# Optimization experiments

Measured on AMD Instinct MI355X. Metric: run time of the kernel, lower is better.

## Reference

```python
import jax, jax.numpy as jnp
import numpy as np

B, H, W, D, C = 2, 128, 128, 8, 64
HEADS, DIM_HEAD = 4, 16
F_IN = C * D            # 512
F_OUT = DIM_HEAD * HEADS * D  # 512


def setup_inputs() -> dict:
    key = jax.random.key(0)
    ks = jax.random.split(key, 8)
    s = 0.02
    return {
        "x_in": jax.random.normal(ks[0], (B, H, W, D, C), dtype=jnp.float32),
        "Wq": jax.random.normal(ks[1], (F_IN, F_OUT), dtype=jnp.float32) * s,
        "Wk": jax.random.normal(ks[2], (F_IN, F_OUT), dtype=jnp.float32) * s,
        "Wv": jax.random.normal(ks[3], (F_IN, F_OUT), dtype=jnp.float32) * s,
        "rescale": jnp.ones((HEADS, 1, 1), dtype=jnp.float32),
        "Wp": jax.random.normal(ks[4], (F_OUT, F_IN), dtype=jnp.float32) * s,
        "bp": jnp.zeros((F_IN,), dtype=jnp.float32),
        "pos_w1": jax.random.normal(ks[5], (C, 1, 3, 3, 3), dtype=jnp.float32) * s,
        "pos_w2": jax.random.normal(ks[6], (C, 1, 3, 3, 3), dtype=jnp.float32) * s,
    }


def _dwconv3d(y, kern, groups):
    # y: [b,c,d,h,w], kern: [c,1,3,3,3] depthwise
    return jax.lax.conv_general_dilated(
        y, kern, window_strides=(1, 1, 1), padding="SAME",
        feature_group_count=groups,
        dimension_numbers=("NCDHW", "OIDHW", "NCDHW"))


def reference(x_in, Wq, Wk, Wv, rescale, Wp, bp, pos_w1, pos_w2):
    b, h, w, d, c = x_in.shape
    heads = rescale.shape[0]
    n = h * w
    x = x_in.reshape(b, n, d * c)
    q_inp = x @ Wq
    k_inp = x @ Wk
    v_inp = x @ Wv

    def split(t):  # [b,n,heads*Dh] -> [b,heads,Dh,n]  (Dh = dim_head*num_frm)
        return t.reshape(b, n, heads, -1).transpose(0, 2, 3, 1)

    q, k, v = split(q_inp), split(k_inp), split(v_inp)
    # L2-normalize along spatial axis n (last dim), torch F.normalize eps=1e-12
    q = q / jnp.maximum(jnp.linalg.norm(q, axis=-1, keepdims=True), 1e-12)
    k = k / jnp.maximum(jnp.linalg.norm(k, axis=-1, keepdims=True), 1e-12)
    # channel attention: [b,heads,Dh,Dh]
    attn = jnp.einsum("bhdn,bhen->bhde", k, q) * rescale
    attn = jax.nn.softmax(attn, axis=-1)
    out = jnp.einsum("bhde,bhen->bhdn", attn, v)  # [b,heads,Dh,n]
    out = out.transpose(0, 3, 1, 2).reshape(b, n, -1)  # [b,n,heads*Dh]
    out_c = (out @ Wp + bp).reshape(b, h, w, d, c)

    # positional branch: depthwise conv3d over [b,c,d,h,w]
    vp = v_inp.reshape(b, h, w, d, c).transpose(0, 4, 3, 1, 2)
    p = _dwconv3d(vp, pos_w1, c)
    p = jax.nn.gelu(p, approximate=False)
    p = _dwconv3d(p, pos_w2, c)
    out_p = p.transpose(0, 3, 4, 2, 1)  # -> [b,h,w,d,c]
    return out_c + out_p
```

## Files before the change

### kernel.cpp

```cpp
#include <hip/hip_runtime.h>
#include <math.h>
#include <stdint.h>


using short8  = __attribute__((ext_vector_type(8))) short;
using f32x4   = __attribute__((ext_vector_type(4))) float;

__device__ __forceinline__ float bf2f(unsigned short u) {
  union { unsigned int i; float f; } v; v.i = ((unsigned int)u) << 16; return v.f;
}
__device__ __forceinline__ unsigned short f2bf(float f) {
  union { float f; unsigned int i; } v; v.f = f;
  unsigned int r = v.i + 0x7fffu + ((v.i >> 16) & 1u);
  return (unsigned short)(r >> 16);
}

__device__ __forceinline__ void g2l16(const void* g, void* l) {
  __builtin_amdgcn_global_load_lds(
      (__attribute__((address_space(1))) void*)(unsigned long long)(uintptr_t)g,
      (__attribute__((address_space(3))) void*)(unsigned int)(uintptr_t)l,
      16, 0, 0);
}

__global__ __launch_bounds__(256) void convert_x(const float* __restrict__ x,
                                                 unsigned short* __restrict__ xb) {
  int i = (blockIdx.x * 256 + threadIdx.x) * 4;
  float4 v = *(const float4*)&x[i];
  ushort4 o;
  o.x = f2bf(v.x); o.y = f2bf(v.y); o.z = f2bf(v.z); o.w = f2bf(v.w);
  *(ushort4*)&xb[i] = o;
}

__global__ __launch_bounds__(256) void prep_w(const float* __restrict__ Wq,
                                              const float* __restrict__ Wk,
                                              const float* __restrict__ Wv,
                                              const float* __restrict__ Wp,
                                              unsigned short* __restrict__ Wcat_t,
                                              unsigned short* __restrict__ Wp_t) {
  __shared__ unsigned short Ls[32 * 36];
  int bid = blockIdx.x;
  int mat = bid >> 8, tile = bid & 255;
  int tr = (tile >> 4) * 32, tc = (tile & 15) * 32;
  const float* src = (mat == 0) ? Wq : (mat == 1) ? Wk : (mat == 2) ? Wv : Wp;
  int t = threadIdx.x;
  int r = t >> 3, c4 = (t & 7) * 4;
  float4 v = *(const float4*)&src[(tr + r) * 512 + tc + c4];
  Ls[(c4 + 0) * 36 + r] = f2bf(v.x);
  Ls[(c4 + 1) * 36 + r] = f2bf(v.y);
  Ls[(c4 + 2) * 36 + r] = f2bf(v.z);
  Ls[(c4 + 3) * 36 + r] = f2bf(v.w);
  __syncthreads();
  int rn = t >> 3, ck4 = (t & 7) * 4;
  ushort4 o;
  o.x = Ls[rn * 36 + ck4 + 0]; o.y = Ls[rn * 36 + ck4 + 1];
  o.z = Ls[rn * 36 + ck4 + 2]; o.w = Ls[rn * 36 + ck4 + 3];
  unsigned short* dst = (mat < 3)
      ? &Wcat_t[(long)(mat * 512 + tc + rn) * 512 + tr + ck4]
      : &Wp_t[(long)(tc + rn) * 512 + tr + ck4];
  *(ushort4*)dst = o;
}

__global__ __launch_bounds__(256, 2) void qk_gram(
    const unsigned short* __restrict__ x_bf,
    const unsigned short* __restrict__ Wcat_t,
    float* __restrict__ Gp, float* __restrict__ ss) {
  __shared__ unsigned short sh[38912];
  unsigned short* As = sh;
  unsigned short* B0 = sh + 8192;
  unsigned short* B1 = sh + 16384;
  const int mt2 = blockIdx.x, h = blockIdx.y, b = blockIdx.z;
  const int t = threadIdx.x;
  const int lane = t & 63, w = t >> 6;
  const int wm = w >> 1, wn = w & 1;
  const int quad = lane >> 4, l16 = lane & 15;
  const int sr = lane >> 3, sc = lane & 7;
  const unsigned short* Bq = Wcat_t + (long)(h * 128) * 512;
  const unsigned short* Bk = Wcat_t + (long)(512 + h * 128) * 512;

  f32x4 g[4][4] = {};

  for (int half = 0; half < 2; half++) {
    const unsigned short* A = x_bf + ((long)b * 16384 + (mt2 * 2 + half) * 128) * 512;
    f32x4 aq[4][4] = {}, ak[4][4] = {};
    for (int k0 = 0; k0 < 512; k0 += 64) {
#pragma unroll
      for (int q = 0; q < 4; q++) {
        int r = q * 32 + w * 8 + sr;
        int ca = (sc ^ sr) * 8;
        g2l16(&A[(long)r * 512 + k0 + ca],  &As[(q * 32 + w * 8) * 64]);
        g2l16(&Bq[(long)r * 512 + k0 + ca], &B0[(q * 32 + w * 8) * 64]);
        g2l16(&Bk[(long)r * 512 + k0 + ca], &B1[(q * 32 + w * 8) * 64]);
      }
      __syncthreads();
#pragma unroll
      for (int kk = 0; kk < 2; kk++) {
        short8 af[4], bq[4], bk[4];
#pragma unroll
        for (int i = 0; i < 4; i++) {
          int r = wm * 64 + i * 16 + l16;
          int s = (kk * 4 + quad) ^ (r & 7);
          af[i] = *(const short8*)&As[r * 64 + s * 8];
        }
#pragma unroll
        for (int j = 0; j < 4; j++) {
          int r = wn * 64 + j * 16 + l16;
          int s = (kk * 4 + quad) ^ (r & 7);
          bq[j] = *(const short8*)&B0[r * 64 + s * 8];
          bk[j] = *(const short8*)&B1[r * 64 + s * 8];
        }
#pragma unroll
        for (int i = 0; i < 4; i++)
#pragma unroll
          for (int j = 0; j < 4; j++) {
            aq[i][j] = __builtin_amdgcn_mfma_f32_16x16x32_bf16(af[i], bq[j], aq[i][j], 0, 0, 0);
            ak[i][j] = __builtin_amdgcn_mfma_f32_16x16x32_bf16(af[i], bk[j], ak[i][j], 0, 0, 0);
          }
      }
      __syncthreads();
    }
    unsigned short* kT = sh;
    unsigned short* qT = sh + 17408;
    float* red = (float*)(sh + 34816);
#pragma unroll
    for (int i = 0; i < 4; i++) {
      int mm = wm * 64 + i * 16 + quad * 4;
#pragma unroll
      for (int j = 0; j < 4; j++) {
        int f = wn * 64 + j * 16 + l16;
        ushort4 oq = { f2bf(aq[i][j][0]), f2bf(aq[i][j][1]), f2bf(aq[i][j][2]), f2bf(aq[i][j][3]) };
        ushort4 ok = { f2bf(ak[i][j][0]), f2bf(ak[i][j][1]), f2bf(ak[i][j][2]), f2bf(ak[i][j][3]) };
        *(ushort4*)&qT[f * 136 + mm] = oq;
        *(ushort4*)&kT[f * 136 + mm] = ok;
      }
    }
    int grp = wm * 4 + quad;
#pragma unroll
    for (int j = 0; j < 4; j++) {
      float pq = 0.f, pk = 0.f;
#pragma unroll
      for (int i = 0; i < 4; i++)
#pragma unroll
        for (int r = 0; r < 4; r++) { pq += aq[i][j][r] * aq[i][j][r]; pk += ak[i][j][r] * ak[i][j][r]; }
      int col = wn * 64 + j * 16 + l16;
      red[grp * 128 + col] = pq;
      red[1024 + grp * 128 + col] = pk;
    }
    __syncthreads();
#pragma unroll
    for (int kk2 = 0; kk2 < 4; kk2++) {
      short8 afk[4], bfq[4];
#pragma unroll
      for (int i = 0; i < 4; i++)
        afk[i] = *(const short8*)&kT[(wm * 64 + i * 16 + l16) * 136 + kk2 * 32 + quad * 8];
#pragma unroll
      for (int j = 0; j < 4; j++)
        bfq[j] = *(const short8*)&qT[(wn * 64 + j * 16 + l16) * 136 + kk2 * 32 + quad * 8];
#pragma unroll
      for (int i = 0; i < 4; i++)
#pragma unroll
        for (int j = 0; j < 4; j++)
          g[i][j] = __builtin_amdgcn_mfma_f32_16x16x32_bf16(afk[i], bfq[j], g[i][j], 0, 0, 0);
    }
    {
      int sel = t >> 7, col = t & 127;
      float s = 0.f;
#pragma unroll
      for (int g2 = 0; g2 < 8; g2++) s += red[sel * 1024 + g2 * 128 + col];
      atomicAdd(&ss[b * 1024 + sel * 512 + h * 128 + col], s);
    }
    __syncthreads();
  }

  float* gp = Gp + (((long)(b * 64 + mt2) * 4 + h) << 14);
#pragma unroll
  for (int i = 0; i < 4; i++) {
    int dd = wm * 64 + i * 16 + quad * 4;
#pragma unroll
    for (int j = 0; j < 4; j++) {
      int e = wn * 64 + j * 16 + l16;
      *(f32x4*)&gp[e * 128 + dd] = g[i][j];
    }
  }
}

__global__ __launch_bounds__(256, 3) void v_gemm(
    const unsigned short* __restrict__ x_bf,
    const unsigned short* __restrict__ Wcat_t,
    unsigned short* __restrict__ v) {
  __shared__ unsigned short As[8192];
  __shared__ unsigned short Bs[8192];
  const int mt = blockIdx.x, nt = blockIdx.y, b = blockIdx.z;
  const int t = threadIdx.x;
  const int lane = t & 63, w = t >> 6;
  const int wm = w >> 1, wn = w & 1;
  const int quad = lane >> 4, l16 = lane & 15;
  const int sr = lane >> 3, sc = lane & 7;
  const unsigned short* A  = x_bf + ((long)b * 16384 + mt * 128) * 512;
  const unsigned short* Bt = Wcat_t + (long)(1024 + nt * 128) * 512;

  f32x4 acc[4][4] = {};
  for (int k0 = 0; k0 < 512; k0 += 64) {
#pragma unroll
    for (int q = 0; q < 4; q++) {
      int r = q * 32 + w * 8 + sr;
      int ca = (sc ^ sr) * 8;
      g2l16(&A[(long)r * 512 + k0 + ca],  &As[(q * 32 + w * 8) * 64]);
      g2l16(&Bt[(long)r * 512 + k0 + ca], &Bs[(q * 32 + w * 8) * 64]);
    }
    __syncthreads();
#pragma unroll
    for (int kk = 0; kk < 2; kk++) {
      short8 af[4], bf[4];
#pragma unroll
      for (int i = 0; i < 4; i++) {
        int r = wm * 64 + i * 16 + l16;
        int s = (kk * 4 + quad) ^ (r & 7);
        af[i] = *(const short8*)&As[r * 64 + s * 8];
      }
#pragma unroll
      for (int j = 0; j < 4; j++) {
        int r = wn * 64 + j * 16 + l16;
        int s = (kk * 4 + quad) ^ (r & 7);
        bf[j] = *(const short8*)&Bs[r * 64 + s * 8];
      }
#pragma unroll
      for (int i = 0; i < 4; i++)
#pragma unroll
        for (int j = 0; j < 4; j++)
          acc[i][j] = __builtin_amdgcn_mfma_f32_16x16x32_bf16(bf[j], af[i], acc[i][j], 0, 0, 0);
    }
    __syncthreads();
  }
  unsigned short* vout = v + ((long)b * 16384 + mt * 128) * 512 + nt * 128;
#pragma unroll
  for (int i = 0; i < 4; i++) {
    long rbase = (long)(wm * 64 + i * 16 + l16) * 512;
#pragma unroll
    for (int j = 0; j < 4; j++) {
      int col = wn * 64 + j * 16 + quad * 4;
      uint2 o;
      o.x = (unsigned)f2bf(acc[i][j][0]) | ((unsigned)f2bf(acc[i][j][1]) << 16);
      o.y = (unsigned)f2bf(acc[i][j][2]) | ((unsigned)f2bf(acc[i][j][3]) << 16);
      *(uint2*)&vout[rbase + col] = o;
    }
  }
}

__global__ __launch_bounds__(256) void reduce_g(const float* __restrict__ Gp,
                                                float* __restrict__ G) {
  int i = blockIdx.x * 256 + threadIdx.x;
  int b = i >> 16, h = (i >> 14) & 3, r = i & 16383;
  const float* p = Gp + (((long)b * 256 + h) << 14) + r;
  float s = 0.f;
#pragma unroll 8
  for (int mtv = 0; mtv < 64; mtv++) s += p[(long)mtv * 65536];
  G[i] = s;
}

__global__ __launch_bounds__(256) void softmax_kernel(const float* __restrict__ Gt,
                                                      const float* __restrict__ ss,
                                                      const float* __restrict__ rescale,
                                                      unsigned short* __restrict__ Abd) {
  __shared__ float L[128 * 129];
  __shared__ float rsq[128];
  __shared__ float rsk[128];
  int h = blockIdx.x, b = blockIdx.y;
  int t = threadIdx.x;
  const float* g = Gt + (long)(b * 4 + h) * 16384;
  if (t < 128) rsq[t] = rsqrtf(fmaxf(ss[b * 1024 + h * 128 + t], 1e-24f));
  else { int d = t - 128; rsk[d] = rsqrtf(fmaxf(ss[b * 1024 + 512 + h * 128 + d], 1e-24f)); }
  __syncthreads();
  float rs = rescale[h];
  for (int i = t; i < 16384; i += 256) {
    int e = i >> 7, d = i & 127;
    L[d * 129 + e] = g[i] * rsk[d] * rsq[e] * rs;
  }
  __syncthreads();
  if (t < 128) {
    float* row = &L[t * 129];
    float mx = -1e30f;
    for (int e = 0; e < 128; e++) mx = fmaxf(mx, row[e]);
    float sum = 0.0f;
    for (int e = 0; e < 128; e++) { float ex = __expf(row[e] - mx); row[e] = ex; sum += ex; }
    float inv = 1.0f / sum;
    long abase = (long)b * 262144;
    for (int e = 0; e < 128; e++)
      Abd[abase + (long)(h * 128 + e) * 512 + h * 128 + t] = f2bf(row[e] * inv);
  }
}

__global__ __launch_bounds__(256, 3) void gemm_lds(
    const unsigned short* __restrict__ A, const unsigned short* __restrict__ Bt,
    unsigned short* __restrict__ C, const float* __restrict__ bias,
    int lda, int ldb, int ldc, int K, long sA, long sB, long sC) {
  __shared__ unsigned short As[128 * 64];
  __shared__ unsigned short Bs[128 * 64];
  const int t = threadIdx.x;
  const int m0 = blockIdx.x * 128, n0 = blockIdx.y * 128;
  A  += (long)blockIdx.z * sA + (long)m0 * lda;
  Bt += (long)blockIdx.z * sB + (long)n0 * ldb;
  C  += (long)blockIdx.z * sC;
  const int lane = t & 63, w = t >> 6;
  const int wm = w >> 1, wn = w & 1;
  const int quad = lane >> 4, l16 = lane & 15;
  const int sr = lane >> 3, sc = lane & 7;

  f32x4 acc[4][4] = {};

  for (int k0 = 0; k0 < K; k0 += 64) {
#pragma unroll
    for (int q = 0; q < 4; q++) {
      int r = q * 32 + w * 8 + sr;
      int ca = (sc ^ sr) * 8;
      g2l16(&A[(long)r * lda + k0 + ca], &As[(q * 32 + w * 8) * 64]);
      g2l16(&Bt[(long)r * ldb + k0 + ca], &Bs[(q * 32 + w * 8) * 64]);
    }
    __syncthreads();
#pragma unroll
    for (int kk = 0; kk < 2; kk++) {
      short8 af[4], bfq[4];
#pragma unroll
      for (int i = 0; i < 4; i++) {
        int r = wm * 64 + i * 16 + l16;
        int s = (kk * 4 + quad) ^ (r & 7);
        af[i] = *(const short8*)&As[r * 64 + s * 8];
      }
#pragma unroll
      for (int j = 0; j < 4; j++) {
        int r = wn * 64 + j * 16 + l16;
        int s = (kk * 4 + quad) ^ (r & 7);
        bfq[j] = *(const short8*)&Bs[r * 64 + s * 8];
      }
#pragma unroll
      for (int i = 0; i < 4; i++)
#pragma unroll
        for (int j = 0; j < 4; j++)
          acc[i][j] = __builtin_amdgcn_mfma_f32_16x16x32_bf16(bfq[j], af[i], acc[i][j], 0, 0, 0);
    }
    __syncthreads();
  }

#pragma unroll
  for (int i = 0; i < 4; i++) {
    long rbase = (long)(m0 + wm * 64 + i * 16 + l16) * ldc;
#pragma unroll
    for (int j = 0; j < 4; j++) {
      int col = n0 + wn * 64 + j * 16 + quad * 4;
      float b0 = 0.f, b1 = 0.f, b2 = 0.f, b3 = 0.f;
      if (bias) { float4 bv = *(const float4*)&bias[col]; b0 = bv.x; b1 = bv.y; b2 = bv.z; b3 = bv.w; }
      uint2 o;
      o.x = (unsigned)f2bf(acc[i][j][0] + b0) | ((unsigned)f2bf(acc[i][j][1] + b1) << 16);
      o.y = (unsigned)f2bf(acc[i][j][2] + b2) | ((unsigned)f2bf(acc[i][j][3] + b3) << 16);
      *(uint2*)&C[rbase + col] = o;
    }
  }
}

template <bool GELU>
__global__ __launch_bounds__(256) void dwconv_kernel(
    const unsigned short* __restrict__ in,
    const float* __restrict__ wgt,
    const unsigned short* __restrict__ addc,
    unsigned short* __restrict__ outb,
    float* __restrict__ outf) {
  __shared__ unsigned short tile[60 * 512];
  __shared__ float wl[27 * 64];
  int wt = blockIdx.x, ht = blockIdx.y, b = blockIdx.z;
  int t = threadIdx.x;
  for (int i = t; i < 1728; i += 256) {
    int c = i / 27, tap = i % 27;
    wl[tap * 64 + c] = wgt[i];
  }
  int h0 = ht * 4, w0 = wt * 8;
  int lg = t & 63;
#pragma unroll 5
  for (int rr = 0; rr < 15; rr++) {
    int row = rr * 4 + (t >> 6);
    int hh = row / 10, ww = row % 10;
    int gh = h0 + hh - 1, gw = w0 + ww - 1;
    uint4 vv = {0u, 0u, 0u, 0u};
    if ((unsigned)gh < 128u && (unsigned)gw < 128u)
      vv = *(const uint4*)&in[((long)(b * 16384 + gh * 128 + gw)) * 512 + lg * 8];
    *(uint4*)&tile[row * 512 + lg * 8] = vv;
  }
  __syncthreads();

  int f0 = lg * 8;
  int d = f0 >> 6, c0 = f0 & 63;
  int pg = t >> 6;
  int pwb = (pg & 1) * 4;
#pragma unroll
  for (int P = 0; P < 2; P++) {
    int ph = P * 2 + (pg >> 1);
    float acc[4][8] = {};
    for (int kd = 0; kd < 3; kd++) {
      int dz = d + kd - 1;
      if ((unsigned)dz >= 8u) continue;
      int fz = dz * 64 + c0;
#pragma unroll
      for (int kh = 0; kh < 3; kh++) {
        float tf[6][8];
#pragma unroll
        for (int cc = 0; cc < 6; cc++) {
          uint4 pv = *(const uint4*)&tile[((ph + kh) * 10 + pwb + cc) * 512 + fz];
          const unsigned short* u = (const unsigned short*)&pv;
#pragma unroll
          for (int j = 0; j < 8; j++) tf[cc][j] = bf2f(u[j]);
        }
#pragma unroll
        for (int kw = 0; kw < 3; kw++) {
          int tap = kd * 9 + kh * 3 + kw;
          float wv[8];
          *(float4*)&wv[0] = *(const float4*)&wl[tap * 64 + c0];
          *(float4*)&wv[4] = *(const float4*)&wl[tap * 64 + c0 + 4];
#pragma unroll
          for (int s = 0; s < 4; s++)
#pragma unroll
            for (int j = 0; j < 8; j++) acc[s][j] += tf[s + kw][j] * wv[j];
        }
      }
    }
#pragma unroll
    for (int s = 0; s < 4; s++) {
      int pw = pwb + s;
      long row = (long)(b * 16384 + (h0 + ph) * 128 + (w0 + pw));
      if (GELU) {
        unsigned short o[8];
#pragma unroll
        for (int j = 0; j < 8; j++) {
          float xg = acc[s][j];
          o[j] = f2bf(0.5f * xg * (1.0f + erff(xg * 0.70710678118654752f)));
        }
        *(uint4*)&outb[row * 512 + f0] = *(uint4*)&o[0];
      } else {
        uint4 av = *(const uint4*)&addc[row * 512 + f0];
        const unsigned short* au = (const unsigned short*)&av;
        float o[8];
#pragma unroll
        for (int j = 0; j < 8; j++) o[j] = acc[s][j] + bf2f(au[j]);
        *(float4*)&outf[row * 512 + f0]     = *(float4*)&o[0];
        *(float4*)&outf[row * 512 + f0 + 4] = *(float4*)&o[4];
      }
    }
  }
}

extern "C" void kernel_launch(void* const* d_in, const int* in_sizes, int n_in,
                              void* d_out, int out_size, void* d_ws, size_t ws_size,
                              hipStream_t stream) {
  const float* x   = (const float*)d_in[0];
  const float* Wq  = (const float*)d_in[1];
  const float* Wk  = (const float*)d_in[2];
  const float* Wv  = (const float*)d_in[3];
  const float* rsc = (const float*)d_in[4];
  const float* Wp  = (const float*)d_in[5];
  const float* bp  = (const float*)d_in[6];
  const float* pw1 = (const float*)d_in[7];
  const float* pw2 = (const float*)d_in[8];
  float* out = (float*)d_out;

  char* ws = (char*)d_ws;
  unsigned short* x_bf   = (unsigned short*)(ws + 0);
  unsigned short* v      = (unsigned short*)(ws + 33554432);
  unsigned short* out_c  = (unsigned short*)(ws + 67108864);
  float*          Gp     = (float*)(ws + 100663296);
  unsigned short* Wcat_t = (unsigned short*)(ws + 167772160);
  unsigned short* Wp_t   = (unsigned short*)(ws + 169345024);
  float*          ss     = (float*)(ws + 169869312);
  float*          G      = (float*)(ws + 169877504);
  unsigned short* Abd    = (unsigned short*)(ws + 170401792);
  unsigned short* Mt     = (unsigned short*)(ws + 171450368);
  unsigned short* p1     = x_bf;

  hipMemsetAsync(ss, 0, 8192, stream);
  hipMemsetAsync(Abd, 0, 1048576, stream);

  convert_x<<<16384, 256, 0, stream>>>(x, x_bf);
  prep_w<<<1024, 256, 0, stream>>>(Wq, Wk, Wv, Wp, Wcat_t, Wp_t);

  qk_gram<<<dim3(64, 4, 2), 256, 0, stream>>>(x_bf, Wcat_t, Gp, ss);
  v_gemm<<<dim3(128, 4, 2), 256, 0, stream>>>(x_bf, Wcat_t, v);

  reduce_g<<<512, 256, 0, stream>>>(Gp, G);
  softmax_kernel<<<dim3(4, 2, 1), 256, 0, stream>>>(G, ss, rsc, Abd);

  gemm_lds<<<dim3(4, 4, 2), 256, 0, stream>>>(
      Wp_t, Abd, Mt, nullptr, 512, 512, 512, 512, 0L, 262144L, 262144L);

  gemm_lds<<<dim3(128, 4, 2), 256, 0, stream>>>(
      v, Mt, out_c, bp, 512, 512, 512, 512,
      (long)16384 * 512, 262144L, (long)16384 * 512);

  dwconv_kernel<true><<<dim3(16, 32, 2), 256, 0, stream>>>(
      v, pw1, nullptr, p1, nullptr);
  dwconv_kernel<false><<<dim3(16, 32, 2), 256, 0, stream>>>(
      p1, pw2, out_c, nullptr, out);
}
```

Before: 351.8 us.

## Double-buffer qk_gram K-loop, use fast GELU approximation, widen convert_x vectors

```diff
diff --git a/kernel.cpp b/kernel.cpp
--- a/kernel.cpp
+++ b/kernel.cpp
@@ -22,13 +22,28 @@
       16, 0, 0);
 }
 
+__device__ __forceinline__ float fast_gelu(float x) {
+  float y = fabsf(x) * 0.70710678118654752f;
+  float t = __builtin_amdgcn_rcpf(1.0f + 0.3275911f * y);
+  float p = ((((1.061405429f * t - 1.453152027f) * t + 1.421413741f) * t
+              - 0.284496736f) * t + 0.254829592f) * t;
+  float er = 1.0f - p * __expf(-y * y);
+  er = copysignf(er, x);
+  return 0.5f * x * (1.0f + er);
+}
+
 __global__ __launch_bounds__(256) void convert_x(const float* __restrict__ x,
                                                  unsigned short* __restrict__ xb) {
-  int i = (blockIdx.x * 256 + threadIdx.x) * 4;
-  float4 v = *(const float4*)&x[i];
-  ushort4 o;
-  o.x = f2bf(v.x); o.y = f2bf(v.y); o.z = f2bf(v.z); o.w = f2bf(v.w);
-  *(ushort4*)&xb[i] = o;
+  int i = (blockIdx.x * 256 + threadIdx.x) * 8;
+  float4 a = *(const float4*)&x[i];
+  float4 b = *(const float4*)&x[i + 4];
+  ushort4 o0, o1;
+  o0.x = f2bf(a.x); o0.y = f2bf(a.y); o0.z = f2bf(a.z); o0.w = f2bf(a.w);
+  o1.x = f2bf(b.x); o1.y = f2bf(b.y); o1.z = f2bf(b.z); o1.w = f2bf(b.w);
+  uint4 o; 
+  o.x = *(unsigned*)&o0.x; o.y = *(unsigned*)&o0.z;
+  o.z = *(unsigned*)&o1.x; o.w = *(unsigned*)&o1.z;
+  *(uint4*)&xb[i] = o;
 }
 
 __global__ __launch_bounds__(256) void prep_w(const float* __restrict__ Wq,
@@ -65,15 +80,12 @@
     const unsigned short* __restrict__ Wcat_t,
     float* __restrict__ Gp, float* __restrict__ ss) {
   __shared__ unsigned short sh[38912];
-  unsigned short* As = sh;
-  unsigned short* B0 = sh + 8192;
-  unsigned short* B1 = sh + 16384;
   const int mt2 = blockIdx.x, h = blockIdx.y, b = blockIdx.z;
   const int t = threadIdx.x;
   const int lane = t & 63, w = t >> 6;
   const int wm = w >> 1, wn = w & 1;
   const int quad = lane >> 4, l16 = lane & 15;
-  const int sr = lane >> 3, sc = lane & 7;
+  const int sr2 = lane >> 2, sc2 = lane & 3;
   const unsigned short* Bq = Wcat_t + (long)(h * 128) * 512;
   const unsigned short* Bk = Wcat_t + (long)(512 + h * 128) * 512;
 
@@ -82,42 +94,55 @@
   for (int half = 0; half < 2; half++) {
     const unsigned short* A = x_bf + ((long)b * 16384 + (mt2 * 2 + half) * 128) * 512;
     f32x4 aq[4][4] = {}, ak[4][4] = {};
-    for (int k0 = 0; k0 < 512; k0 += 64) {
-#pragma unroll
-      for (int q = 0; q < 4; q++) {
-        int r = q * 32 + w * 8 + sr;
-        int ca = (sc ^ sr) * 8;
-        g2l16(&A[(long)r * 512 + k0 + ca],  &As[(q * 32 + w * 8) * 64]);
-        g2l16(&Bq[(long)r * 512 + k0 + ca], &B0[(q * 32 + w * 8) * 64]);
-        g2l16(&Bk[(long)r * 512 + k0 + ca], &B1[(q * 32 + w * 8) * 64]);
-      }
+
+    auto stage = [&](int k0, int d) {
+      unsigned short* Sa = sh + d * 12288;
+      unsigned short* Sq = Sa + 4096;
+      unsigned short* Sk = Sa + 8192;
+#pragma unroll
+      for (int q = 0; q < 2; q++) {
+        int r = q * 64 + w * 16 + sr2;
+        int ca = (sc2 ^ (sr2 & 3)) * 8;
+        long off = (long)r * 512 + k0 + ca;
+        int ldsb = (q * 64 + w * 16) * 32;
+        g2l16(&A[off],  &Sa[ldsb]);
+        g2l16(&Bq[off], &Sq[ldsb]);
+        g2l16(&Bk[off], &Sk[ldsb]);
+      }
+    };
+
+    stage(0, 0);
+    __syncthreads();
+    for (int ks = 0; ks < 16; ks++) {
+      int d = ks & 1;
+      if (ks < 15) stage((ks + 1) * 32, d ^ 1);
+      const unsigned short* Sa = sh + d * 12288;
+      const unsigned short* Sq = Sa + 4096;
+      const unsigned short* Sk = Sa + 8192;
+      short8 af[4], bq4[4], bk4[4];
+#pragma unroll
+      for (int i = 0; i < 4; i++) {
+        int r = wm * 64 + i * 16 + l16;
+        int s = quad ^ (r & 3);
+        af[i] = *(const short8*)&Sa[r * 32 + s * 8];
+      }
+#pragma unroll
+      for (int j = 0; j < 4; j++) {
+        int r = wn * 64 + j * 16 + l16;
+        int s = quad ^ (r & 3);
+        bq4[j] = *(const short8*)&Sq[r * 32 + s * 8];
+        bk4[j] = *(const short8*)&Sk[r * 32 + s * 8];
+      }
+#pragma unroll
+      for (int i = 0; i < 4; i++)
+#pragma unroll
+        for (int j = 0; j < 4; j++) {
+          aq[i][j] = __builtin_amdgcn_mfma_f32_16x16x32_bf16(af[i], bq4[j], aq[i][j], 0, 0, 0);
+          ak[i][j] = __builtin_amdgcn_mfma_f32_16x16x32_bf16(af[i], bk4[j], ak[i][j], 0, 0, 0);
+        }
       __syncthreads();
-#pragma unroll
-      for (int kk = 0; kk < 2; kk++) {
-        short8 af[4], bq[4], bk[4];
-#pragma unroll
-        for (int i = 0; i < 4; i++) {
-          int r = wm * 64 + i * 16 + l16;
-          int s = (kk * 4 + quad) ^ (r & 7);
-          af[i] = *(const short8*)&As[r * 64 + s * 8];
-        }
-#pragma unroll
-        for (int j = 0; j < 4; j++) {
-          int r = wn * 64 + j * 16 + l16;
-          int s = (kk * 4 + quad) ^ (r & 7);
-          bq[j] = *(const short8*)&B0[r * 64 + s * 8];
-          bk[j] = *(const short8*)&B1[r * 64 + s * 8];
-        }
-#pragma unroll
-        for (int i = 0; i < 4; i++)
-#pragma unroll
-          for (int j = 0; j < 4; j++) {
-            aq[i][j] = __builtin_amdgcn_mfma_f32_16x16x32_bf16(af[i], bq[j], aq[i][j], 0, 0, 0);
-            ak[i][j] = __builtin_amdgcn_mfma_f32_16x16x32_bf16(af[i], bk[j], ak[i][j], 0, 0, 0);
-          }
-      }
-      __syncthreads();
-    }
+    }
+
     unsigned short* kT = sh;
     unsigned short* qT = sh + 17408;
     float* red = (float*)(sh + 34816);
@@ -427,10 +452,7 @@
       if (GELU) {
         unsigned short o[8];
 #pragma unroll
-        for (int j = 0; j < 8; j++) {
-          float xg = acc[s][j];
-          o[j] = f2bf(0.5f * xg * (1.0f + erff(xg * 0.70710678118654752f)));
-        }
+        for (int j = 0; j < 8; j++) o[j] = f2bf(fast_gelu(acc[s][j]));
         *(uint4*)&outb[row * 512 + f0] = *(uint4*)&o[0];
       } else {
         uint4 av = *(const uint4*)&addc[row * 512 + f0];
@@ -475,7 +497,7 @@
   hipMemsetAsync(ss, 0, 8192, stream);
   hipMemsetAsync(Abd, 0, 1048576, stream);
 
-  convert_x<<<16384, 256, 0, stream>>>(x, x_bf);
+  convert_x<<<8192, 256, 0, stream>>>(x, x_bf);
   prep_w<<<1024, 256, 0, stream>>>(Wq, Wk, Wv, Wp, Wcat_t, Wp_t);
 
   qk_gram<<<dim3(64, 4, 2), 256, 0, stream>>>(x_bf, Wcat_t, Gp, ss);
```

Result: no change. 349.0 us (-0.8%).
